# Kernel optimization log

Hardware: AMD Instinct MI355X
Metric: run time of the kernel (lower is better)

## Reference

```python
import jax, jax.numpy as jnp
import numpy as np

B, S, HID = 2, 1024, 1024
H, P, D = 16, 2, 64
SCALE = 1.0 / np.sqrt(D)


def setup_inputs() -> dict:
    key = jax.random.key(0)
    ks = jax.random.split(key, 9)
    hidden_states = jax.random.normal(ks[0], (B, S, HID), dtype=jnp.float32)
    w_std = 0.02
    Wq = jax.random.normal(ks[1], (HID, HID), dtype=jnp.float32) * w_std
    Wk = jax.random.normal(ks[2], (HID, HID), dtype=jnp.float32) * w_std
    Wv = jax.random.normal(ks[3], (HID, HID), dtype=jnp.float32) * w_std
    Wo = jax.random.normal(ks[4], (HID, HID), dtype=jnp.float32) * w_std
    # alpha_* initialized as identity over heads, broadcast over pseudo dim, plus noise
    ident = jnp.broadcast_to(jnp.eye(H, dtype=jnp.float32)[:, :, None], (H, H, P))
    alpha_q = ident + 0.01 * jax.random.normal(ks[5], (H, H, P), dtype=jnp.float32)
    alpha_k = ident + 0.01 * jax.random.normal(ks[6], (H, H, P), dtype=jnp.float32)
    alpha_v = ident + 0.01 * jax.random.normal(ks[7], (H, H, P), dtype=jnp.float32)
    # collapse: (H, H*P), one-hot picking pseudo-head 0 of each head, plus noise
    collapse = jnp.zeros((H, H * P), dtype=jnp.float32)
    hi = jnp.arange(H)
    collapse = collapse.at[hi, hi * P].set(1.0)
    collapse = collapse + 0.01 * jax.random.normal(ks[8], (H, H * P), dtype=jnp.float32)
    return {"hidden_states": hidden_states, "Wq": Wq, "Wk": Wk, "Wv": Wv, "Wo": Wo,
            "alpha_q": alpha_q, "alpha_k": alpha_k, "alpha_v": alpha_v, "collapse": collapse}


def _iha_forward(x, Wq, Wk, Wv, Wo, alpha_q, alpha_k, alpha_v, collapse):
    b, s, _ = x.shape
    # projections (torch F.linear: x @ W^T), split into heads -> (b, H, s, D)
    def proj(W):
        return jnp.einsum('bse,fe->bsf', x, W).reshape(b, s, H, D).transpose(0, 2, 1, 3)
    q, k, v = proj(Wq), proj(Wk), proj(Wv)
    # head mixing: mhp,bmnd->bhpnd then merge pseudo into virtual seq (b,H,s*P,D)
    def mix_merge(alpha, t):
        t = jnp.einsum('mhp,bmnd->bhpnd', alpha, t)
        return t.transpose(0, 1, 3, 2, 4).reshape(b, H, s * P, D)
    q, k, v = mix_merge(alpha_q, q), mix_merge(alpha_k, k), mix_merge(alpha_v, v)
    # causal SDPA over virtual positions
    sv = s * P
    scores = jnp.einsum('bhqd,bhkd->bhqk', q, k) * jnp.asarray(SCALE, x.dtype)
    vpos = jnp.arange(sv)
    causal = vpos[:, None] >= vpos[None, :]
    scores = jnp.where(causal, scores, jnp.asarray(-jnp.inf, x.dtype))
    probs = jax.nn.softmax(scores, axis=-1)
    attn = jnp.einsum('bhqk,bhkd->bhqd', probs, v)  # (b, H, sv, D)
    # collapse pseudo heads: (b,H,s,P,D) -> (b,s,H*P,D) -> einsum with collapse
    attn = attn.reshape(b, H, s, P, D).transpose(0, 2, 1, 3, 4).reshape(b, s, H * P, D)
    attn = jnp.einsum('ho,bnod->bhnd', collapse, attn)  # (b, H, s, D)
    attn = attn.transpose(0, 2, 1, 3).reshape(b, s, HID)
    return jnp.einsum('bse,fe->bsf', attn, Wo)


def reference(hidden_states, Wq, Wk, Wv, Wo, alpha_q, alpha_k, alpha_v, collapse):
    return _iha_forward(hidden_states, Wq, Wk, Wv, Wo, alpha_q, alpha_k, alpha_v, collapse)
```

## Files before the change

kernel.cpp:

```cpp
#include <hip/hip_runtime.h>
#include <hip/hip_bf16.h>

#define B_    2
#define S_    1024
#define HID_  1024
#define H_    16
#define P_    2
#define D_    64
#define SV_   2048
#define NBH_  32
#define SCALE_LOG2E 0.18033688f

typedef __attribute__((ext_vector_type(8))) short short8;
typedef __attribute__((ext_vector_type(4))) float f32x4;

#if __has_builtin(__builtin_amdgcn_exp2f)
#define EXP2(x) __builtin_amdgcn_exp2f(x)
#else
#define EXP2(x) exp2f(x)
#endif

__device__ __forceinline__ unsigned short f2bf(float f) {
  union { float f; unsigned u; } v; v.f = f;
  unsigned r = v.u + 0x7fffu + ((v.u >> 16) & 1u);
  return (unsigned short)(r >> 16);
}
__device__ __forceinline__ unsigned pack_bf2(float a, float b) {
  __hip_bfloat162 h = __float22bfloat162_rn(make_float2(a, b));
  unsigned u; __builtin_memcpy(&u, &h, 4);
  return u;
}

__global__ __launch_bounds__(256) void cast_f32_bf16(
    const float* __restrict__ src, unsigned short* __restrict__ dst, int n4) {
  int i = blockIdx.x * blockDim.x + threadIdx.x;
  int stride = gridDim.x * blockDim.x;
  for (; i < n4; i += stride) {
    float4 v = ((const float4*)src)[i];
    ushort4 o;
    o.x = f2bf(v.x); o.y = f2bf(v.y); o.z = f2bf(v.z); o.w = f2bf(v.w);
    ((ushort4*)dst)[i] = o;
  }
}

__global__ __launch_bounds__(256) void weff_kernel(
    const float* __restrict__ Wq, const float* __restrict__ Wk,
    const float* __restrict__ Wv,
    const float* __restrict__ aq, const float* __restrict__ ak,
    const float* __restrict__ av,
    unsigned short* __restrict__ Weff) {
  __shared__ float Al[16][32];
  const int d = blockIdx.x;
  const int t = blockIdx.y;
  const float* W = (t == 0) ? Wq : ((t == 1) ? Wk : Wv);
  const float* A = (t == 0) ? aq : ((t == 1) ? ak : av);
  const int tid = threadIdx.x;
  for (int idx = tid; idx < 512; idx += 256) Al[idx >> 5][idx & 31] = A[idx];
  __syncthreads();
  const int e = tid * 4;
  float wr[16][4];
#pragma unroll
  for (int m = 0; m < 16; ++m) {
    float4 v = *(const float4*)(W + (size_t)(m * 64 + d) * 1024 + e);
    wr[m][0] = v.x; wr[m][1] = v.y; wr[m][2] = v.z; wr[m][3] = v.w;
  }
  for (int hp = 0; hp < 32; ++hp) {
    float acc0 = 0.f, acc1 = 0.f, acc2 = 0.f, acc3 = 0.f;
#pragma unroll
    for (int m = 0; m < 16; ++m) {
      float al = Al[m][hp];
      acc0 += al * wr[m][0]; acc1 += al * wr[m][1];
      acc2 += al * wr[m][2]; acc3 += al * wr[m][3];
    }
    int r = (hp >> 1) * 128 + (hp & 1) * 64 + d;
    ushort4 ov;
    ov.x = f2bf(acc0); ov.y = f2bf(acc1); ov.z = f2bf(acc2); ov.w = f2bf(acc3);
    *(ushort4*)(Weff + ((size_t)t * 2048 + r) * 1024 + e) = ov;
  }
}

__global__ __launch_bounds__(256) void woeff_kernel(
    const float* __restrict__ Wo, const float* __restrict__ coll,
    unsigned short* __restrict__ Woeff) {
  __shared__ float wrow[1024];
  __shared__ float cl[512];
  const int f = blockIdx.x;
  const int tid = threadIdx.x;
  for (int idx = tid; idx < 512; idx += 256) cl[idx] = coll[idx];
  for (int idx = tid; idx < 1024; idx += 256) wrow[idx] = Wo[(size_t)f * 1024 + idx];
  __syncthreads();
  for (int idx = tid; idx < 2048; idx += 256) {
    int o = idx >> 6, d = idx & 63;
    float acc = 0.f;
#pragma unroll
    for (int h = 0; h < 16; ++h) acc += wrow[h * 64 + d] * cl[h * 32 + o];
    Woeff[(size_t)f * 2048 + idx] = f2bf(acc);
  }
}

__global__ __launch_bounds__(256) void qkv_gemm(
    const unsigned short* __restrict__ Xb,
    const unsigned short* __restrict__ Weff,
    unsigned short* __restrict__ Qd, unsigned short* __restrict__ Kd,
    unsigned short* __restrict__ Vd) {
  __shared__ unsigned short As[2][128 * 32];
  __shared__ unsigned short Bs[2][128 * 32];
  const int K = 1024;
  const int t = threadIdx.x;
  const int wave = t >> 6, lane = t & 63, lrow = lane & 15, quad = lane >> 4;
  const int wm = wave >> 1, wn = wave & 1;
  const int row0 = blockIdx.x * 128;
  const int col0 = blockIdx.y * 128;
  const int z = blockIdx.z;
  const unsigned short* Ap = (z == 2) ? (Weff + (size_t)2 * 2048 * 1024) : Xb;
  const unsigned short* Bp = (z == 2) ? Xb : (Weff + (size_t)z * 2048 * 1024);

  const int r16 = lane >> 2;
  const int gc = (lane & 3) * 8;

  auto stage = [&](int k0, int buf) {
#pragma unroll
    for (int j = 0; j < 2; ++j) {
      const int cc = wave * 2 + j;
      const unsigned short* ga = Ap + (size_t)(row0 + cc * 16 + r16) * K + k0 + gc;
      __builtin_amdgcn_global_load_lds(
          (const __attribute__((address_space(1))) unsigned int*)ga,
          (__attribute__((address_space(3))) unsigned int*)(&As[buf][cc * 512]), 16, 0, 0);
      const unsigned short* gb = Bp + (size_t)(col0 + cc * 16 + r16) * K + k0 + gc;
      __builtin_amdgcn_global_load_lds(
          (const __attribute__((address_space(1))) unsigned int*)gb,
          (__attribute__((address_space(3))) unsigned int*)(&Bs[buf][cc * 512]), 16, 0, 0);
    }
  };

  f32x4 acc[4][4];
#pragma unroll
  for (int mi = 0; mi < 4; ++mi)
#pragma unroll
    for (int ni = 0; ni < 4; ++ni) acc[mi][ni] = (f32x4){0.f, 0.f, 0.f, 0.f};

  const int niter = K >> 5;
  stage(0, 0);

  for (int it = 0; it < niter; ++it) {
    const int buf = it & 1;
    if (it + 1 < niter) {
      stage((it + 1) * 32, buf ^ 1);
      asm volatile("s_waitcnt vmcnt(4)" ::: "memory");
    } else {
      asm volatile("s_waitcnt vmcnt(0)" ::: "memory");
    }
    asm volatile("s_barrier" ::: "memory");

    short8 af[4], bfr[4];
#pragma unroll
    for (int mi = 0; mi < 4; ++mi)
      af[mi] = *(const short8*)(&As[buf][(wm * 64 + mi * 16 + lrow) * 32 + quad * 8]);
#pragma unroll
    for (int ni = 0; ni < 4; ++ni)
      bfr[ni] = *(const short8*)(&Bs[buf][(wn * 64 + ni * 16 + lrow) * 32 + quad * 8]);
#pragma unroll
    for (int mi = 0; mi < 4; ++mi)
#pragma unroll
      for (int ni = 0; ni < 4; ++ni)
        acc[mi][ni] = __builtin_amdgcn_mfma_f32_16x16x32_bf16(af[mi], bfr[ni],
                                                              acc[mi][ni], 0, 0, 0);

    asm volatile("s_barrier" ::: "memory");
  }

#pragma unroll
  for (int mi = 0; mi < 4; ++mi) {
#pragma unroll
    for (int ni = 0; ni < 4; ++ni) {
#pragma unroll
      for (int i = 0; i < 4; ++i) {
        int grow = row0 + wm * 64 + mi * 16 + quad * 4 + i;
        int gcol = col0 + wn * 64 + ni * 16 + lrow;
        float val = acc[mi][ni][i];
        if (z != 2) {
          int b = grow >> 10, n = grow & 1023;
          int h = gcol >> 7, p = (gcol >> 6) & 1, d = gcol & 63;
          unsigned short* dst = (z == 0) ? Qd : Kd;
          dst[((size_t)((b * 16 + h) * 2048) + n * 2 + p) * 64 + d] = f2bf(val);
        } else {
          int h = grow >> 7, p = (grow >> 6) & 1, d = grow & 63;
          int b = gcol >> 10, n = gcol & 1023;
          Vd[((size_t)((b * 16 + h) * 64 + d)) * 2048 + n * 2 + p] = f2bf(val);
        }
      }
    }
  }
}

__global__ __launch_bounds__(256) void gemm64(
    const unsigned short* __restrict__ A,
    const unsigned short* __restrict__ Bbase,
    int M, int N, int K, float* __restrict__ Cf) {
  __shared__ unsigned short As[2][64 * 32];
  __shared__ unsigned short Bs[2][128 * 32];
  const int t = threadIdx.x;
  const int wave = t >> 6, lane = t & 63, lrow = lane & 15, quad = lane >> 4;
  const int row0 = blockIdx.x * 64;
  const int col0 = blockIdx.y * 128;

  const int r16 = lane >> 2;
  const int gc = (lane & 3) * 8;

  auto stage = [&](int k0, int buf) {
    const unsigned short* ga = A + (size_t)(row0 + wave * 16 + r16) * K + k0 + gc;
    __builtin_amdgcn_global_load_lds(
        (const __attribute__((address_space(1))) unsigned int*)ga,
        (__attribute__((address_space(3))) unsigned int*)(&As[buf][wave * 512]), 16, 0, 0);
#pragma unroll
    for (int j = 0; j < 2; ++j) {
      const int cc = wave * 2 + j;
      const unsigned short* gb = Bbase + (size_t)(col0 + cc * 16 + r16) * K + k0 + gc;
      __builtin_amdgcn_global_load_lds(
          (const __attribute__((address_space(1))) unsigned int*)gb,
          (__attribute__((address_space(3))) unsigned int*)(&Bs[buf][cc * 512]), 16, 0, 0);
    }
  };

  f32x4 acc[4][2];
#pragma unroll
  for (int mi = 0; mi < 4; ++mi)
#pragma unroll
    for (int ni = 0; ni < 2; ++ni) acc[mi][ni] = (f32x4){0.f, 0.f, 0.f, 0.f};

  const int niter = K >> 5;
  stage(0, 0);

  for (int it = 0; it < niter; ++it) {
    const int buf = it & 1;
    if (it + 1 < niter) {
      stage((it + 1) * 32, buf ^ 1);
      asm volatile("s_waitcnt vmcnt(3)" ::: "memory");
    } else {
      asm volatile("s_waitcnt vmcnt(0)" ::: "memory");
    }
    asm volatile("s_barrier" ::: "memory");

    short8 af[4], bfr[2];
#pragma unroll
    for (int mi = 0; mi < 4; ++mi)
      af[mi] = *(const short8*)(&As[buf][(mi * 16 + lrow) * 32 + quad * 8]);
#pragma unroll
    for (int ni = 0; ni < 2; ++ni)
      bfr[ni] = *(const short8*)(&Bs[buf][(wave * 32 + ni * 16 + lrow) * 32 + quad * 8]);
#pragma unroll
    for (int mi = 0; mi < 4; ++mi)
#pragma unroll
      for (int ni = 0; ni < 2; ++ni)
        acc[mi][ni] = __builtin_amdgcn_mfma_f32_16x16x32_bf16(af[mi], bfr[ni],
                                                              acc[mi][ni], 0, 0, 0);

    asm volatile("s_barrier" ::: "memory");
  }

#pragma unroll
  for (int mi = 0; mi < 4; ++mi)
#pragma unroll
    for (int ni = 0; ni < 2; ++ni)
#pragma unroll
      for (int i = 0; i < 4; ++i) {
        int grow = row0 + mi * 16 + quad * 4 + i;
        int gcol = col0 + wave * 32 + ni * 16 + lrow;
        Cf[(size_t)grow * N + gcol] = acc[mi][ni][i];
      }
}

__global__ __launch_bounds__(256, 4) void attn_kernel(
    const unsigned short* __restrict__ Qv, const unsigned short* __restrict__ Kv,
    const unsigned short* __restrict__ Vt, unsigned short* __restrict__ Aov) {
  __shared__ unsigned short Ks[2][4096];
  __shared__ unsigned short Vs[2][4096];
  __shared__ unsigned short Plds[4][1024];
  const int bh = blockIdx.x;
  const int yy = blockIdx.y;
  const int qt = (yy < 16) ? yy : (47 - yy);
  const int t = threadIdx.x;
  const int w = t >> 6, lane = t & 63, lq = lane & 15, quad = lane >> 4;
  const int l3 = lq & 7;

  const unsigned short* Qh = Qv + (size_t)bh * SV_ * D_;
  const unsigned short* Kh = Kv + (size_t)bh * SV_ * D_;
  const unsigned short* Vh = Vt + (size_t)bh * D_ * SV_;

  const int qrow = qt * 64 + w * 16 + lq;
  short8 bq0 = *(const short8*)(Qh + (size_t)qrow * 64 + quad * 8);
  short8 bq1 = *(const short8*)(Qh + (size_t)qrow * 64 + 32 + quad * 8);

  const int sg = (lane & 7) ^ ((lane >> 3) & 7);
  const int r0 = w * 16 + (lane >> 3);
  const unsigned short* Kg0 = Kh + r0 * 64 + sg * 8;
  const unsigned short* Vg0 = Vh + (size_t)r0 * SV_ + sg * 8;
  const int lds0 = w * 1024;
  const int lds1 = lds0 + 512;

  auto stage = [&](int kt) {
    const int buf = kt & 1;
    const unsigned short* kg = Kg0 + kt * 4096;
    const unsigned short* vg = Vg0 + kt * 64;
    __builtin_amdgcn_global_load_lds(
        (const __attribute__((address_space(1))) unsigned int*)kg,
        (__attribute__((address_space(3))) unsigned int*)(&Ks[buf][lds0]), 16, 0, 0);
    __builtin_amdgcn_global_load_lds(
        (const __attribute__((address_space(1))) unsigned int*)(kg + 8 * 64),
        (__attribute__((address_space(3))) unsigned int*)(&Ks[buf][lds1]), 16, 0, 0);
    __builtin_amdgcn_global_load_lds(
        (const __attribute__((address_space(1))) unsigned int*)vg,
        (__attribute__((address_space(3))) unsigned int*)(&Vs[buf][lds0]), 16, 0, 0);
    __builtin_amdgcn_global_load_lds(
        (const __attribute__((address_space(1))) unsigned int*)(vg + (size_t)8 * SV_),
        (__attribute__((address_space(3))) unsigned int*)(&Vs[buf][lds1]), 16, 0, 0);
  };

  unsigned short* Pw = Plds[w];

  float l_sum = 0.f;
  f32x4 o_acc[4];
#pragma unroll
  for (int nd = 0; nd < 4; ++nd) o_acc[nd] = (f32x4){0.f, 0.f, 0.f, 0.f};

  const int nt = qt + 1;
  stage(0);

  for (int kt = 0; kt < nt; ++kt) {
    const int buf = kt & 1;
    if (kt + 1 < nt) {
      stage(kt + 1);
      asm volatile("s_waitcnt vmcnt(4)" ::: "memory");
    } else {
      asm volatile("s_waitcnt vmcnt(0)" ::: "memory");
    }
    asm volatile("s_barrier" ::: "memory");

    const unsigned short* Kb = Ks[buf];
    short8 ka[4][2];
#pragma unroll
    for (int t4 = 0; t4 < 4; ++t4)
#pragma unroll
      for (int c = 0; c < 2; ++c)
        ka[t4][c] = *(const short8*)(Kb + (t4 * 16 + lq) * 64 + (((c * 4 + quad) ^ l3) * 8));

    f32x4 s[4];
#pragma unroll
    for (int t4 = 0; t4 < 4; ++t4) {
      f32x4 z = (f32x4){0.f, 0.f, 0.f, 0.f};
      z = __builtin_amdgcn_mfma_f32_16x16x32_bf16(ka[t4][0], bq0, z, 0, 0, 0);
      s[t4] = __builtin_amdgcn_mfma_f32_16x16x32_bf16(ka[t4][1], bq1, z, 0, 0, 0);
    }

    const bool diag = (kt == qt);
    const int kc0 = kt * 64 + quad * 4;
    float rs = 0.f;
#pragma unroll
    for (int t4 = 0; t4 < 4; ++t4) {
      float p[4];
#pragma unroll
      for (int i = 0; i < 4; ++i) {
        float e = EXP2(s[t4][i] * SCALE_LOG2E);
        if (diag) e = (kc0 + t4 * 16 + i > qrow) ? 0.f : e;
        p[i] = e;
        rs += e;
      }
      uint2 dw;
      dw.x = pack_bf2(p[0], p[1]);
      dw.y = pack_bf2(p[2], p[3]);
      const int cg = t4 * 2 + (quad >> 1);
      *(uint2*)(Pw + lq * 64 + ((cg ^ l3) * 8) + (quad & 1) * 4) = dw;
    }
    l_sum += rs;

    const unsigned short* Vb = Vs[buf];
#pragma unroll
    for (int kh = 0; kh < 2; ++kh) {
      short8 bp = *(const short8*)(Pw + lq * 64 + (((kh * 4 + quad) ^ l3) * 8));
#pragma unroll
      for (int nd = 0; nd < 4; ++nd) {
        short8 va = *(const short8*)(Vb + (nd * 16 + lq) * 64 + (((kh * 4 + quad) ^ l3) * 8));
        o_acc[nd] = __builtin_amdgcn_mfma_f32_16x16x32_bf16(va, bp, o_acc[nd], 0, 0, 0);
      }
    }

    asm volatile("s_barrier" ::: "memory");
  }

  l_sum += __shfl_xor(l_sum, 16);
  l_sum += __shfl_xor(l_sum, 32);

  const int b = bh >> 4, h = bh & 15;
  const float inv = 1.0f / l_sum;
  const int n = qrow >> 1, p = qrow & 1;
  unsigned short* dst = Aov + ((size_t)(b * 1024 + n)) * 2048 + (h * 2 + p) * 64;
#pragma unroll
  for (int nd = 0; nd < 4; ++nd) {
    uint2 dw;
    dw.x = pack_bf2(o_acc[nd][0] * inv, o_acc[nd][1] * inv);
    dw.y = pack_bf2(o_acc[nd][2] * inv, o_acc[nd][3] * inv);
    *(uint2*)(dst + nd * 16 + quad * 4) = dw;
  }
}

extern "C" void kernel_launch(void* const* d_in, const int* in_sizes, int n_in,
                              void* d_out, int out_size, void* d_ws, size_t ws_size,
                              hipStream_t stream) {
  (void)in_sizes; (void)n_in; (void)out_size; (void)ws_size;
  const float* x    = (const float*)d_in[0];
  const float* Wq   = (const float*)d_in[1];
  const float* Wk   = (const float*)d_in[2];
  const float* Wv   = (const float*)d_in[3];
  const float* Wo   = (const float*)d_in[4];
  const float* aq   = (const float*)d_in[5];
  const float* ak   = (const float*)d_in[6];
  const float* av   = (const float*)d_in[7];
  const float* coll = (const float*)d_in[8];
  float* out = (float*)d_out;

  char* ws = (char*)d_ws;
  const size_t MB = 1024 * 1024;
  unsigned short* Xb    = (unsigned short*)(ws);
  unsigned short* Woeff = (unsigned short*)(ws + 4 * MB);
  unsigned short* Weff  = (unsigned short*)(ws + 8 * MB);
  unsigned short* Qv    = (unsigned short*)(ws + 20 * MB);
  unsigned short* Kv    = (unsigned short*)(ws + 28 * MB);
  unsigned short* Vt    = (unsigned short*)(ws + 36 * MB);
  unsigned short* Aov   = (unsigned short*)(ws + 8 * MB);

  cast_f32_bf16<<<dim3(1024), dim3(256), 0, stream>>>(x, Xb, (B_ * S_ * HID_) / 4);
  weff_kernel<<<dim3(64, 3), dim3(256), 0, stream>>>(Wq, Wk, Wv, aq, ak, av, Weff);
  qkv_gemm<<<dim3(16, 16, 3), dim3(256), 0, stream>>>(Xb, Weff, Qv, Kv, Vt);
  attn_kernel<<<dim3(32, 32), dim3(256), 0, stream>>>(Qv, Kv, Vt, Aov);
  woeff_kernel<<<dim3(1024), dim3(256), 0, stream>>>(Wo, coll, Woeff);
  gemm64<<<dim3(32, 8), dim3(256), 0, stream>>>(
      Aov, Woeff, 2048, 1024, 2048, out);
}
```

Before: 207.5 us.

## Rewrite QKV GEMM with 256x256 tiles, swizzled LDS and interleaved staging

Replaces the 128x128 QKV projection GEMM with a 512-thread 256x256 tile kernel using K-steps of 64. It XOR-swizzles the LDS layout to avoid bank conflicts, and staggers the global-to-LDS loads of the next tile across four MFMA sub-phases, with raised wave priority during MFMA. The aim is more data reuse per LDS load and better overlap of memory and compute. In exchange the grid shrinks to 192 blocks, which can underfill the GPU, and the 128 KB of LDS per block limits occupancy.

```diff
diff --git a/kernel.cpp b/kernel.cpp
--- a/kernel.cpp
+++ b/kernel.cpp
@@ -98,84 +98,144 @@
   }
 }
 
-__global__ __launch_bounds__(256) void qkv_gemm(
+__global__ __launch_bounds__(512) void qkv_gemm256(
     const unsigned short* __restrict__ Xb,
     const unsigned short* __restrict__ Weff,
     unsigned short* __restrict__ Qd, unsigned short* __restrict__ Kd,
     unsigned short* __restrict__ Vd) {
-  __shared__ unsigned short As[2][128 * 32];
-  __shared__ unsigned short Bs[2][128 * 32];
-  const int K = 1024;
+  __shared__ unsigned short As[2][256 * 64];
+  __shared__ unsigned short Bs[2][256 * 64];
+  constexpr int K = 1024;
+  constexpr int NT = 16;
   const int t = threadIdx.x;
   const int wave = t >> 6, lane = t & 63, lrow = lane & 15, quad = lane >> 4;
-  const int wm = wave >> 1, wn = wave & 1;
-  const int row0 = blockIdx.x * 128;
-  const int col0 = blockIdx.y * 128;
+  const int wm = wave >> 2, wn = wave & 3;
   const int z = blockIdx.z;
+  const int row0 = blockIdx.x * 256, col0 = blockIdx.y * 256;
   const unsigned short* Ap = (z == 2) ? (Weff + (size_t)2 * 2048 * 1024) : Xb;
   const unsigned short* Bp = (z == 2) ? Xb : (Weff + (size_t)z * 2048 * 1024);
 
-  const int r16 = lane >> 2;
-  const int gc = (lane & 3) * 8;
-
-  auto stage = [&](int k0, int buf) {
+  const int srow8 = lane >> 3;
+  const int sslot = (lane & 7) ^ srow8;
+
+  auto stageHT = [&](const unsigned short* __restrict__ gsrc,
+                     unsigned short* __restrict__ ldsbase,
+                     int half, int kt, int trow0) {
 #pragma unroll
     for (int j = 0; j < 2; ++j) {
-      const int cc = wave * 2 + j;
-      const unsigned short* ga = Ap + (size_t)(row0 + cc * 16 + r16) * K + k0 + gc;
+      const int rloc = half * 128 + wave * 16 + j * 8;
+      const unsigned short* g =
+          gsrc + (size_t)(trow0 + rloc + srow8) * K + kt * 64 + sslot * 8;
       __builtin_amdgcn_global_load_lds(
-          (const __attribute__((address_space(1))) unsigned int*)ga,
-          (__attribute__((address_space(3))) unsigned int*)(&As[buf][cc * 512]), 16, 0, 0);
-      const unsigned short* gb = Bp + (size_t)(col0 + cc * 16 + r16) * K + k0 + gc;
-      __builtin_amdgcn_global_load_lds(
-          (const __attribute__((address_space(1))) unsigned int*)gb,
-          (__attribute__((address_space(3))) unsigned int*)(&Bs[buf][cc * 512]), 16, 0, 0);
+          (const __attribute__((address_space(1))) unsigned int*)g,
+          (__attribute__((address_space(3))) unsigned int*)(ldsbase + rloc * 64),
+          16, 0, 0);
     }
   };
 
-  f32x4 acc[4][4];
-#pragma unroll
-  for (int mi = 0; mi < 4; ++mi)
+  f32x4 acc[8][4];
+#pragma unroll
+  for (int mi = 0; mi < 8; ++mi)
 #pragma unroll
     for (int ni = 0; ni < 4; ++ni) acc[mi][ni] = (f32x4){0.f, 0.f, 0.f, 0.f};
 
-  const int niter = K >> 5;
-  stage(0, 0);
-
-  for (int it = 0; it < niter; ++it) {
-    const int buf = it & 1;
-    if (it + 1 < niter) {
-      stage((it + 1) * 32, buf ^ 1);
-      asm volatile("s_waitcnt vmcnt(4)" ::: "memory");
-    } else {
-      asm volatile("s_waitcnt vmcnt(0)" ::: "memory");
-    }
-    asm volatile("s_barrier" ::: "memory");
-
-    short8 af[4], bfr[4];
-#pragma unroll
-    for (int mi = 0; mi < 4; ++mi)
-      af[mi] = *(const short8*)(&As[buf][(wm * 64 + mi * 16 + lrow) * 32 + quad * 8]);
-#pragma unroll
-    for (int ni = 0; ni < 4; ++ni)
-      bfr[ni] = *(const short8*)(&Bs[buf][(wn * 64 + ni * 16 + lrow) * 32 + quad * 8]);
-#pragma unroll
-    for (int mi = 0; mi < 4; ++mi)
-#pragma unroll
-      for (int ni = 0; ni < 4; ++ni)
-        acc[mi][ni] = __builtin_amdgcn_mfma_f32_16x16x32_bf16(af[mi], bfr[ni],
-                                                              acc[mi][ni], 0, 0, 0);
-
-    asm volatile("s_barrier" ::: "memory");
-  }
-
-#pragma unroll
-  for (int mi = 0; mi < 4; ++mi) {
+  stageHT(Ap, &As[0][0], 0, 0, row0);
+  stageHT(Ap, &As[0][0], 1, 0, row0);
+  stageHT(Bp, &Bs[0][0], 0, 0, col0);
+  stageHT(Bp, &Bs[0][0], 1, 0, col0);
+  stageHT(Bp, &Bs[1][0], 0, 1, col0);
+  stageHT(Bp, &Bs[1][0], 1, 1, col0);
+  asm volatile("s_waitcnt vmcnt(4)" ::: "memory");
+  asm volatile("s_barrier" ::: "memory");
+
+  const int swz = lrow & 7;
+
+#define LDA(mi, ks)                                                         \
+  (*(const short8*)(Ab + (wm * 128 + (mi)*16 + lrow) * 64 +                 \
+                    ((((ks)*4 + quad) ^ swz) * 8)))
+
+#define MFMA_PAIR(mA, mB, a00, a01, a10, a11)                               \
+  _Pragma("unroll") for (int ni = 0; ni < 4; ++ni) {                        \
+    acc[mA][ni] = __builtin_amdgcn_mfma_f32_16x16x32_bf16(                  \
+        a00, bfrag[ni][0], acc[mA][ni], 0, 0, 0);                           \
+    acc[mA][ni] = __builtin_amdgcn_mfma_f32_16x16x32_bf16(                  \
+        a01, bfrag[ni][1], acc[mA][ni], 0, 0, 0);                           \
+    acc[mB][ni] = __builtin_amdgcn_mfma_f32_16x16x32_bf16(                  \
+        a10, bfrag[ni][0], acc[mB][ni], 0, 0, 0);                           \
+    acc[mB][ni] = __builtin_amdgcn_mfma_f32_16x16x32_bf16(                  \
+        a11, bfrag[ni][1], acc[mB][ni], 0, 0, 0);                           \
+  }
+
+  for (int kt = 0; kt < NT; ++kt) {
+    const int buf = kt & 1, nbuf = buf ^ 1;
+    const unsigned short* __restrict__ Ab = &As[buf][0];
+    const unsigned short* __restrict__ Bb = &Bs[buf][0];
+
+    short8 bfrag[4][2];
+    {
+#pragma unroll
+      for (int ni = 0; ni < 4; ++ni) {
+        const int R = wn * 64 + ni * 16 + lrow;
+#pragma unroll
+        for (int ks = 0; ks < 2; ++ks)
+          bfrag[ni][ks] =
+              *(const short8*)(Bb + R * 64 + (((ks * 4 + quad) ^ swz) * 8));
+      }
+      short8 a00 = LDA(0, 0), a01 = LDA(0, 1), a10 = LDA(1, 0), a11 = LDA(1, 1);
+      if (kt + 1 < NT) stageHT(Ap, &As[nbuf][0], 0, kt + 1, row0);
+      asm volatile("s_barrier" ::: "memory");
+      asm volatile("s_waitcnt lgkmcnt(0)" ::: "memory");
+      __builtin_amdgcn_s_setprio(1);
+      MFMA_PAIR(0, 1, a00, a01, a10, a11)
+      __builtin_amdgcn_s_setprio(0);
+      asm volatile("s_barrier" ::: "memory");
+    }
+    {
+      short8 a00 = LDA(2, 0), a01 = LDA(2, 1), a10 = LDA(3, 0), a11 = LDA(3, 1);
+      if (kt + 1 < NT) stageHT(Ap, &As[nbuf][0], 1, kt + 1, row0);
+      asm volatile("s_barrier" ::: "memory");
+      asm volatile("s_waitcnt lgkmcnt(0)" ::: "memory");
+      __builtin_amdgcn_s_setprio(1);
+      MFMA_PAIR(2, 3, a00, a01, a10, a11)
+      __builtin_amdgcn_s_setprio(0);
+      asm volatile("s_barrier" ::: "memory");
+    }
+    {
+      short8 a00 = LDA(4, 0), a01 = LDA(4, 1), a10 = LDA(5, 0), a11 = LDA(5, 1);
+      if (kt + 2 < NT) stageHT(Bp, &Bs[buf][0], 0, kt + 2, col0);
+      asm volatile("s_barrier" ::: "memory");
+      asm volatile("s_waitcnt lgkmcnt(0)" ::: "memory");
+      __builtin_amdgcn_s_setprio(1);
+      MFMA_PAIR(4, 5, a00, a01, a10, a11)
+      __builtin_amdgcn_s_setprio(0);
+      asm volatile("s_barrier" ::: "memory");
+    }
+    {
+      short8 a00 = LDA(6, 0), a01 = LDA(6, 1), a10 = LDA(7, 0), a11 = LDA(7, 1);
+      if (kt + 2 < NT) stageHT(Bp, &Bs[buf][0], 1, kt + 2, col0);
+      asm volatile("s_barrier" ::: "memory");
+      asm volatile("s_waitcnt lgkmcnt(0)" ::: "memory");
+      __builtin_amdgcn_s_setprio(1);
+      MFMA_PAIR(6, 7, a00, a01, a10, a11)
+      __builtin_amdgcn_s_setprio(0);
+      if (kt + 2 < NT) {
+        asm volatile("s_waitcnt vmcnt(4)" ::: "memory");
+      } else {
+        asm volatile("s_waitcnt vmcnt(0)" ::: "memory");
+      }
+      asm volatile("s_barrier" ::: "memory");
+    }
+  }
+#undef LDA
+#undef MFMA_PAIR
+
+#pragma unroll
+  for (int mi = 0; mi < 8; ++mi) {
 #pragma unroll
     for (int ni = 0; ni < 4; ++ni) {
 #pragma unroll
       for (int i = 0; i < 4; ++i) {
-        int grow = row0 + wm * 64 + mi * 16 + quad * 4 + i;
+        int grow = row0 + wm * 128 + mi * 16 + quad * 4 + i;
         int gcol = col0 + wn * 64 + ni * 16 + lrow;
         float val = acc[mi][ni][i];
         if (z != 2) {
@@ -430,7 +490,7 @@
 
   cast_f32_bf16<<<dim3(1024), dim3(256), 0, stream>>>(x, Xb, (B_ * S_ * HID_) / 4);
   weff_kernel<<<dim3(64, 3), dim3(256), 0, stream>>>(Wq, Wk, Wv, aq, ak, av, Weff);
-  qkv_gemm<<<dim3(16, 16, 3), dim3(256), 0, stream>>>(Xb, Weff, Qv, Kv, Vt);
+  qkv_gemm256<<<dim3(8, 8, 3), dim3(512), 0, stream>>>(Xb, Weff, Qv, Kv, Vt);
   attn_kernel<<<dim3(32, 32), dim3(256), 0, stream>>>(Qv, Kv, Vt, Aov);
   woeff_kernel<<<dim3(1024), dim3(256), 0, stream>>>(Wo, coll, Woeff);
   gemm64<<<dim3(32, 8), dim3(256), 0, stream>>>(
```

Measured after the change: 211.6 us. +2.0%, slower.
